# Performance work log

Hardware: AMD Instinct MI355X
Metric: run time of the kernel (lower is better)

The kernel has to match this reference:

```python
import jax, jax.numpy as jnp
import numpy as np

H = 256                      # latent_channels = LSTM hidden
OC = [32, 64, 64, 128]       # out_channels per mesh level
V = [5023, 1256, 314, 79, 20]  # vertex counts per level (fine -> coarse)
L = 9                        # spiral length
T = 64                       # audio frames (batch for decoder)


def setup_inputs() -> dict:
    key = jax.random.key(0)
    ks = iter(jax.random.split(key, 80))
    f32 = jnp.float32

    def nrm(shape, fan_in):
        return jax.random.normal(next(ks), shape, f32) * (1.0 / np.sqrt(fan_in))

    inp = {}
    inp['audio'] = jax.random.normal(next(ks), (T, 768), f32)
    inp['actor'] = jax.random.normal(next(ks), (V[0], 3), f32)

    # 5-layer bidirectional LSTM; layer 0 input 768, layers 1-4 input 2H
    inp['lstm_Wih0'] = nrm((2, 4 * H, 768), 768)
    inp['lstm_Whh0'] = nrm((2, 4 * H, H), H)
    inp['lstm_b0'] = jnp.zeros((2, 4 * H), f32)
    inp['lstm_Wih'] = nrm((4, 2, 4 * H, 2 * H), 2 * H)
    inp['lstm_Whh'] = nrm((4, 2, 4 * H, H), H)
    inp['lstm_b'] = jnp.zeros((4, 2, 4 * H), f32)

    # decoder entry fc: 2*latent -> num_vert * oc[-1]
    inp['fc_W'] = nrm((V[4] * OC[3], 2 * H), 2 * H)
    inp['fc_b'] = jnp.zeros((V[4] * OC[3],), f32)

    # SpiralConv weights (torch Linear layout: [out, in*L])
    inp['conv3_W'] = nrm((128, 128 * L), 128 * L); inp['conv3_b'] = jnp.zeros((128,), f32)
    inp['conv2_W'] = nrm((64, 128 * L), 128 * L);  inp['conv2_b'] = jnp.zeros((64,), f32)
    inp['conv1_W'] = nrm((64, 64 * L), 64 * L);    inp['conv1_b'] = jnp.zeros((64,), f32)
    inp['conv0_W'] = nrm((32, 64 * L), 64 * L);    inp['conv0_b'] = jnp.zeros((32,), f32)
    inp['head_W'] = nrm((3, 32 * L), 32 * L);      inp['head_b'] = jnp.zeros((3,), f32)

    # spiral indices per level: [V_j, L] with values in [0, V_j)
    for j in range(4):
        inp[f'idx{j}'] = jax.random.randint(next(ks), (V[j], L), 0, V[j], jnp.int32)

    # up_transform[j] sparse [V_j, V_{j+1}], ~3 nnz per row (COO)
    for j in range(4):
        nnz = 3 * V[j]
        inp[f'rows{j}'] = jnp.repeat(jnp.arange(V[j], dtype=jnp.int32), 3)
        inp[f'cols{j}'] = jax.random.randint(next(ks), (nnz,), 0, V[j + 1], jnp.int32)
        inp[f'vals{j}'] = jax.random.uniform(next(ks), (nnz,), f32) / 3.0
    return inp


def _lstm_dir(x, Wih, Whh, b, reverse):
    # x: [T, Din]; torch gate order i, f, g, o
    def step(carry, xt):
        h, c = carry
        g = Wih @ xt + Whh @ h + b            # [4H]
        i, f, gg, o = jnp.split(g, 4)
        c = jax.nn.sigmoid(f) * c + jax.nn.sigmoid(i) * jnp.tanh(gg)
        h = jax.nn.sigmoid(o) * jnp.tanh(c)
        return (h, c), h
    init = (jnp.zeros((H,), x.dtype), jnp.zeros((H,), x.dtype))
    _, hs = jax.lax.scan(step, init, x, reverse=reverse)
    return hs  # [T, H], aligned with input order


def _bilstm(x, Wih, Whh, b):
    hf = _lstm_dir(x, Wih[0], Whh[0], b[0], False)
    hb = _lstm_dir(x, Wih[1], Whh[1], b[1], True)
    return jnp.concatenate([hf, hb], axis=-1)  # [T, 2H]


def _pool(x, rows, cols, vals, n_out):
    # sparse up-transform: out[t, r] = sum_nnz vals * x[t, cols]
    g = x[:, cols, :] * vals[None, :, None]                       # [T, nnz, C]
    return jax.ops.segment_sum(g.swapaxes(0, 1), rows, num_segments=n_out).swapaxes(0, 1)


def _spiral(x, idx, W, b):
    # gather fixed spiral neighborhoods then dense linear
    g = x[:, idx, :].reshape(x.shape[0], idx.shape[0], -1)        # [T, V, L*C]
    return g @ W.T + b


def reference(audio, actor, lstm_Wih0, lstm_Whh0, lstm_b0, lstm_Wih, lstm_Whh, lstm_b,
              fc_W, fc_b, conv3_W, conv3_b, conv2_W, conv2_b, conv1_W, conv1_b,
              conv0_W, conv0_b, head_W, head_b,
              vals3, vals2, vals1, vals0,
              idx0, idx1, idx2, idx3,
              rows3, cols3, rows2, cols2, rows1, cols1, rows0, cols0):
    # audio embedding: 5-layer bidirectional LSTM (batch = 1)
    z = _bilstm(audio, lstm_Wih0, lstm_Whh0, lstm_b0)
    for l in range(4):
        z = _bilstm(z, lstm_Wih[l], lstm_Whh[l], lstm_b[l])       # [T, 2H]

    # decode
    x = (z @ fc_W.T + fc_b).reshape(z.shape[0], V[4], OC[3])      # [T, 20, 128]
    x = jax.nn.elu(_spiral(_pool(x, rows3, cols3, vals3, V[3]), idx3, conv3_W, conv3_b))
    x = jax.nn.elu(_spiral(_pool(x, rows2, cols2, vals2, V[2]), idx2, conv2_W, conv2_b))
    x = jax.nn.elu(_spiral(_pool(x, rows1, cols1, vals1, V[1]), idx1, conv1_W, conv1_b))
    x = jax.nn.elu(_spiral(_pool(x, rows0, cols0, vals0, V[0]), idx0, conv0_W, conv0_b))
    x = _spiral(x, idx0, head_W, head_b)                          # [T, 5023, 3]
    return x + actor[None]
```

## Files before the change

kernel.cpp:

```cpp
#include <hip/hip_runtime.h>
#include <hip/hip_bf16.h>

typedef __attribute__((ext_vector_type(8))) __bf16 bf16x8;
typedef __attribute__((ext_vector_type(4))) float  f32x4;
typedef __attribute__((ext_vector_type(4))) int    i32x4;

#define SCOPE_AGENT __HIP_MEMORY_SCOPE_AGENT

static __device__ __forceinline__ f32x4 mfma16(bf16x8 a, bf16x8 b, f32x4 c) {
    return __builtin_amdgcn_mfma_f32_16x16x32_bf16(a, b, c, 0, 0, 0);
}
static __device__ __forceinline__ i32x4 mfma_i8(i32x4 a, i32x4 b, i32x4 c) {
    return __builtin_amdgcn_mfma_i32_16x16x64_i8(a, b, c, 0, 0, 0);
}
static __device__ __forceinline__ float sigm(float x)  { return 1.0f / (1.0f + __expf(-x)); }
static __device__ __forceinline__ float tanh_(float x) { return 1.0f - 2.0f / (__expf(2.0f * x) + 1.0f); }

static __device__ __forceinline__ bf16x8 cvt8(const float* __restrict__ p) {
    const float4* q = (const float4*)p;
    float4 a = q[0], b = q[1];
    bf16x8 r;
    r[0] = (__bf16)a.x; r[1] = (__bf16)a.y; r[2] = (__bf16)a.z; r[3] = (__bf16)a.w;
    r[4] = (__bf16)b.x; r[5] = (__bf16)b.y; r[6] = (__bf16)b.z; r[7] = (__bf16)b.w;
    return r;
}
static __device__ __forceinline__ void signal_add(unsigned int* p) {
    __hip_atomic_fetch_add(p, 1u, __ATOMIC_RELEASE, SCOPE_AGENT);
}
template <int SLP>
static __device__ __forceinline__ void wait_eq(unsigned int* p, unsigned int v) {
    while (__hip_atomic_load(p, __ATOMIC_RELAXED, SCOPE_AGENT) != v)
        __builtin_amdgcn_s_sleep(SLP);
    (void)__hip_atomic_load(p, __ATOMIC_ACQUIRE, SCOPE_AGENT);
}
union g4u { unsigned long long q; __bf16 h[4]; };

#define ZBUF_OFF   1024
#define GX_OFF     132096
#define CONVW_OFF  66560
#define ARENA_A    621248
#define ARENA_B    21195456
#define WHHQ_BOFF  11534336
#define SWP_BOFF   14155776

__global__ __launch_bounds__(256) void precvt_whh(
    const float* __restrict__ Whh0, const float* __restrict__ WhhL,
    signed char* __restrict__ WhhQ, float* __restrict__ swp)
{
    const int g  = blockIdx.x * 4 + (threadIdx.x >> 6);
    const int dl = g >> 10;
    const int r  = g & 1023;
    const int lane = threadIdx.x & 63;
    const float* src = (dl < 2 ? Whh0 + (size_t)dl * 262144
                               : WhhL + (size_t)(dl - 2) * 262144) + (size_t)r * 256;
    float4 v = *(const float4*)(src + lane * 4);
    float am = fmaxf(fmaxf(fabsf(v.x), fabsf(v.y)), fmaxf(fabsf(v.z), fabsf(v.w)));
    #pragma unroll
    for (int m = 1; m < 64; m <<= 1) am = fmaxf(am, __shfl_xor(am, m));
    const float inv = am > 0.f ? 127.f / am : 0.f;
    int q0 = __float2int_rn(v.x * inv), q1 = __float2int_rn(v.y * inv);
    int q2 = __float2int_rn(v.z * inv), q3 = __float2int_rn(v.w * inv);
    unsigned pk = (q0 & 255) | ((q1 & 255) << 8) | ((q2 & 255) << 16) | ((q3 & 255) << 24);
    const int gate = r >> 8, cell = r & 255;
    const int m  = cell * 4 + gate;
    const int ln = m & 15, mt = m >> 4;
    const int k  = lane * 4;
    const int kc = k >> 6, quad = (k >> 4) & 3, j = k & 15;
    size_t addr = ((((size_t)dl * 64 + mt) * 4 + kc) * 64 + (quad * 16 + ln)) * 16 + j;
    *(unsigned*)(WhhQ + addr) = pk;
    if (lane == 0) swp[(size_t)dl * 1024 + cell * 4 + gate] = am / 127.f;
}

__global__ __launch_bounds__(256) void precvt_dec(
    const float* __restrict__ fcW, const float* __restrict__ c3W,
    const float* __restrict__ c2W, const float* __restrict__ c1W,
    const float* __restrict__ c0W, const float* __restrict__ hW,
    __bf16* __restrict__ fcWb, __bf16* __restrict__ convWb)
{
    int f = (blockIdx.x * 256 + threadIdx.x) * 4;
    if (f >= 1588064) return;
    const float* src; int off; __bf16* dst; int doff;
    if (f < 1310720) { src = fcW; off = f; dst = fcWb; doff = f; }
    else {
        int g = f - 1310720; dst = convWb; doff = g;
        if (g < 147456)      { src = c3W; off = g; }
        else if (g < 221184) { src = c2W; off = g - 147456; }
        else if (g < 258048) { src = c1W; off = g - 221184; }
        else if (g < 276480) { src = c0W; off = g - 258048; }
        else                 { src = hW;  off = g - 276480; }
    }
    float4 v = *(const float4*)(src + off);
    g4u u;
    u.h[0] = (__bf16)v.x; u.h[1] = (__bf16)v.y; u.h[2] = (__bf16)v.z; u.h[3] = (__bf16)v.w;
    *(unsigned long long*)(dst + doff) = u.q;
}

__global__ __launch_bounds__(512) __attribute__((amdgpu_waves_per_eu(2, 2)))
void lstm_fused(
    const float* __restrict__ audio,
    const float* __restrict__ Wih0,
    const float* __restrict__ WihL,
    const signed char* __restrict__ WhhQ,
    const float* __restrict__ swp,
    const float* __restrict__ b0, const float* __restrict__ bL,
    unsigned short* __restrict__ Gx_g,
    unsigned int* __restrict__ flags,
    unsigned short* __restrict__ zbuf)
{
    const int bid = blockIdx.x;
    const int tid = threadIdx.x;
    const int wave = tid >> 6, lane = tid & 63, ln = lane & 15, quad = lane >> 4;

    __shared__ __align__(16) signed char    hq[2][256];
    __shared__ __align__(16) unsigned short gx_l[16384];

    if (bid < 16) {
        const int dir = bid >> 3, sub = bid & 7;
        const int gmt = sub * 8 + wave;
        const int m_a = gmt * 16 + ln;
        const int r_a = (m_a & 3) * 256 + (m_a >> 2);
        unsigned short* GxO = Gx_g + (size_t)dir * 65536;

        {
            const float* Wih_l = Wih0 + (size_t)dir * 786432;
            const float* b_l   = b0 + (size_t)dir * 1024;
            bf16x8 afr[24];
            #pragma unroll
            for (int kc = 0; kc < 24; ++kc)
                afr[kc] = cvt8(Wih_l + (size_t)r_a * 768 + kc * 32 + quad * 8);
            float bv[4];
            #pragma unroll
            for (int reg = 0; reg < 4; ++reg) {
                const int m_row = gmt * 16 + quad * 4 + reg;
                bv[reg] = b_l[(m_row & 3) * 256 + (m_row >> 2)];
            }
            for (int ii = 0; ii < 4; ++ii) {
                const int nt = dir ? 3 - ii : ii;
                const int t  = nt * 16 + ln;
                f32x4 acA = (f32x4){0.f, 0.f, 0.f, 0.f};
                f32x4 acB = (f32x4){0.f, 0.f, 0.f, 0.f};
                #pragma unroll
                for (int kc = 0; kc < 24; kc += 2) {
                    acA = mfma16(afr[kc],
                                 cvt8(audio + (size_t)t * 768 + kc * 32 + quad * 8), acA);
                    acB = mfma16(afr[kc + 1],
                                 cvt8(audio + (size_t)t * 768 + (kc + 1) * 32 + quad * 8), acB);
                }
                f32x4 acc = acA + acB;
                #pragma unroll
                for (int reg = 0; reg < 4; ++reg) {
                    const int m_row = gmt * 16 + quad * 4 + reg;
                    __bf16 v = (__bf16)(acc[reg] + bv[reg]);
                    GxO[(size_t)t * 1024 + m_row] = __builtin_bit_cast(unsigned short, v);
                }
                __syncthreads();
                if (tid == 0) { __threadfence(); signal_add(&flags[(0 * 2 + dir) * 4 + nt]); }
            }
        }

        for (int l = 1; l < 5; ++l) {
            const float* Wih_l = WihL + (size_t)((l - 1) * 2 + dir) * 524288;
            const float* b_l   = bL + (size_t)((l - 1) * 2 + dir) * 1024;
            bf16x8 afr[16];
            #pragma unroll
            for (int kc = 0; kc < 16; ++kc)
                afr[kc] = cvt8(Wih_l + (size_t)r_a * 512 + kc * 32 + quad * 8);
            float bv[4];
            #pragma unroll
            for (int reg = 0; reg < 4; ++reg) {
                const int m_row = gmt * 16 + quad * 4 + reg;
                bv[reg] = b_l[(m_row & 3) * 256 + (m_row >> 2)];
            }
            if (tid == 0) wait_eq<4>(&flags[48 + (l - 1)], 2u);
            __syncthreads();
            const __bf16* zp = (const __bf16*)(zbuf + (size_t)((l - 1) & 1) * 32768);

            for (int ii = 0; ii < 4; ++ii) {
                const int nt = dir ? 3 - ii : ii;
                const int t  = nt * 16 + ln;
                f32x4 acA = (f32x4){0.f, 0.f, 0.f, 0.f};
                f32x4 acB = (f32x4){0.f, 0.f, 0.f, 0.f};
                #pragma unroll
                for (int kc = 0; kc < 16; kc += 2) {
                    acA = mfma16(afr[kc],
                                 *(const bf16x8*)(zp + (size_t)t * 512 + kc * 32 + quad * 8), acA);
                    acB = mfma16(afr[kc + 1],
                                 *(const bf16x8*)(zp + (size_t)t * 512 + (kc + 1) * 32 + quad * 8), acB);
                }
                f32x4 acc = acA + acB;
                #pragma unroll
                for (int reg = 0; reg < 4; ++reg) {
                    const int m_row = gmt * 16 + quad * 4 + reg;
                    __bf16 v = (__bf16)(acc[reg] + bv[reg]);
                    GxO[(size_t)t * 1024 + m_row] = __builtin_bit_cast(unsigned short, v);
                }
                __syncthreads();
                if (tid == 0) { __threadfence(); signal_add(&flags[(l * 2 + dir) * 4 + nt]); }
            }
        }
    } else {
        const int dir = bid - 16;
        const unsigned short* Gx_d = Gx_g + (size_t)dir * 65536;
        const bool owner = (ln < 8);
        const int cell = wave * 32 + ln * 4 + quad;
        const int gcell = owner ? cell : 0;
        const i32x4 czero = (i32x4){0, 0, 0, 0};

        for (int l = 0; l < 5; ++l) {
            const int dl = l * 2 + dir;
            i32x4 wf[8][4];
            const i32x4* wb = (const i32x4*)(WhhQ + (size_t)dl * 262144);
            #pragma unroll
            for (int i = 0; i < 8; ++i)
                #pragma unroll
                for (int kc = 0; kc < 4; ++kc)
                    wf[i][kc] = wb[(size_t)(((wave * 8 + i) * 4 + kc)) * 64 + lane];
            float sc0 = 0.f, sc1 = 0.f, sc2 = 0.f, sc3 = 0.f;
            if (owner) {
                float4 s4 = *(const float4*)(swp + (size_t)dl * 1024 + cell * 4);
                const float f = 1.f / 127.f;
                sc0 = s4.x * f; sc1 = s4.y * f; sc2 = s4.z * f; sc3 = s4.w * f;
            }
            if (tid < 64) ((unsigned int*)hq[0])[tid] = 0;
            float cst = 0.f;
            unsigned short* zl = zbuf + (size_t)(l & 1) * 32768;
            const int gxbase = (l * 2 + dir) * 4;

            for (int s = 0; s < 64; ++s) {
                if ((s & 15) == 0) {
                    const int nt = dir ? 3 - (s >> 4) : (s >> 4);
                    if (tid == 0) wait_eq<1>(&flags[gxbase + nt], 8u);
                    __syncthreads();
                    const float4* src = (const float4*)(Gx_d + (size_t)nt * 16384);
                    float4* dst = (float4*)gx_l;
                    #pragma unroll
                    for (int i = 0; i < 4; ++i) dst[i * 512 + tid] = src[i * 512 + tid];
                    __syncthreads();
                }
                const int t = dir ? (63 - s) : s;
                const int tl = t & 15;
                const int cur = s & 1, nxt = cur ^ 1;
                g4u gx;
                gx.q = *(const unsigned long long*)&gx_l[tl * 1024 + gcell * 4];
                i32x4 acc[8];
                {
                    i32x4 b0v = *(const i32x4*)&hq[cur][quad * 16];
                    #pragma unroll
                    for (int i = 0; i < 8; ++i) acc[i] = mfma_i8(wf[i][0], b0v, czero);
                }
                #pragma unroll
                for (int kc = 1; kc < 4; ++kc) {
                    i32x4 b = *(const i32x4*)&hq[cur][kc * 64 + quad * 16];
                    #pragma unroll
                    for (int i = 0; i < 8; ++i) acc[i] = mfma_i8(wf[i][kc], b, acc[i]);
                }
                i32x4 a = acc[0];
                #pragma unroll
                for (int j = 1; j < 8; ++j) if (ln == j) a = acc[j];
                if (owner) {
                    float gi = (float)a[0] * sc0 + (float)gx.h[0];
                    float gf = (float)a[1] * sc1 + (float)gx.h[1];
                    float gg = (float)a[2] * sc2 + (float)gx.h[2];
                    float go = (float)a[3] * sc3 + (float)gx.h[3];
                    cst = sigm(gf) * cst + sigm(gi) * tanh_(gg);
                    float h = sigm(go) * tanh_(cst);
                    int q = __float2int_rn(h * 127.f);
                    hq[nxt][cell] = (signed char)q;
                    __bf16 zv = (__bf16)((float)q * (1.f / 127.f));
                    zl[(size_t)t * 512 + dir * 256 + cell] =
                        __builtin_bit_cast(unsigned short, zv);
                }
                __syncthreads();
            }
            if (tid == 0) { __threadfence(); signal_add(&flags[48 + l]); }
        }
    }
}

__global__ __launch_bounds__(256) void fc_kernel(
    const __bf16* __restrict__ zb, const __bf16* __restrict__ W,
    const float* __restrict__ bb, __bf16* __restrict__ out)
{
    const int tid = threadIdx.x;
    const int wave = tid >> 6, lane = tid & 63, ln = lane & 15, quad = lane >> 4;
    const int nbase = blockIdx.x * 64;
    f32x4 acc[4];
    #pragma unroll
    for (int nt = 0; nt < 4; nt++) acc[nt] = (f32x4){0.f, 0.f, 0.f, 0.f};
    #pragma unroll 2
    for (int kc = 0; kc < 16; kc++) {
        const int k0 = kc * 32 + quad * 8;
        bf16x8 a = *(const bf16x8*)(zb + (size_t)(wave * 16 + ln) * 512 + k0);
        #pragma unroll
        for (int nt = 0; nt < 4; nt++) {
            bf16x8 b = *(const bf16x8*)(W + (size_t)(nbase + nt * 16 + ln) * 512 + k0);
            acc[nt] = mfma16(a, b, acc[nt]);
        }
    }
    #pragma unroll
    for (int nt = 0; nt < 4; nt++) {
        const int n = nbase + nt * 16 + ln;
        const float bv = bb[n];
        #pragma unroll
        for (int reg = 0; reg < 4; reg++) {
            const int t = wave * 16 + quad * 4 + reg;
            out[(size_t)((n >> 7) * 64 + t) * 128 + (n & 127)] = (__bf16)(acc[nt][reg] + bv);
        }
    }
}

template <int C>
__global__ __launch_bounds__(256) void pool_kernel(
    const __bf16* __restrict__ in, __bf16* __restrict__ out,
    const int* __restrict__ cols, const float* __restrict__ vals, int V)
{
    const int P = 64 * C / 8;
    const int gid = blockIdx.x * 256 + threadIdx.x;
    if (gid >= V * P) return;
    const int r = gid / P;
    const int rem = gid - r * P;
    float acc[8] = {0.f, 0.f, 0.f, 0.f, 0.f, 0.f, 0.f, 0.f};
    #pragma unroll
    for (int s = 0; s < 3; s++) {
        const int col = cols[3 * r + s];
        const float vv = vals[3 * r + s];
        bf16x8 x = *(const bf16x8*)(in + (size_t)col * 64 * C + rem * 8);
        #pragma unroll
        for (int e = 0; e < 8; e++) acc[e] += vv * (float)x[e];
    }
    bf16x8 ov;
    #pragma unroll
    for (int e = 0; e < 8; e++) ov[e] = (__bf16)acc[e];
    *(bf16x8*)(out + (size_t)r * 64 * C + rem * 8) = ov;
}

template <int CIN, int COUT>
__global__ __launch_bounds__(256) void conv_kernel(
    const __bf16* __restrict__ in, __bf16* __restrict__ out,
    const int* __restrict__ idx, const __bf16* __restrict__ W,
    const float* __restrict__ bias)
{
    constexpr int K = 9 * CIN;
    constexpr int NT = COUT / 16;
    constexpr int NKC = K / 32;
    const int v = blockIdx.x;
    const int tid = threadIdx.x;
    const int wave = tid >> 6, lane = tid & 63, ln = lane & 15, quad = lane >> 4;
    __shared__ int sIdx[9];
    if (tid < 9) sIdx[tid] = idx[v * 9 + tid];
    __syncthreads();
    f32x4 acc[NT];
    #pragma unroll
    for (int nt = 0; nt < NT; nt++) acc[nt] = (f32x4){0.f, 0.f, 0.f, 0.f};
    const int tt = wave * 16 + ln;
    for (int kc = 0; kc < NKC; kc++) {
        const int k0 = kc * 32;
        const int l = k0 / CIN;
        const int c = (k0 & (CIN - 1)) + quad * 8;
        const int row = sIdx[l];
        bf16x8 a = *(const bf16x8*)(in + ((size_t)row * 64 + tt) * CIN + c);
        #pragma unroll
        for (int nt = 0; nt < NT; nt++) {
            bf16x8 b = *(const bf16x8*)(W + (size_t)(nt * 16 + ln) * K + k0 + quad * 8);
            acc[nt] = mfma16(a, b, acc[nt]);
        }
    }
    #pragma unroll
    for (int nt = 0; nt < NT; nt++) {
        const int n = nt * 16 + ln;
        const float bv = bias[n];
        #pragma unroll
        for (int reg = 0; reg < 4; reg++) {
            const int t = wave * 16 + quad * 4 + reg;
            float val = acc[nt][reg] + bv;
            val = val > 0.f ? val : (__expf(val) - 1.f);
            out[((size_t)v * 64 + t) * COUT + n] = (__bf16)val;
        }
    }
}

__global__ __launch_bounds__(256) void head_kernel(
    const __bf16* __restrict__ in, float* __restrict__ out,
    const int* __restrict__ idx, const __bf16* __restrict__ W,
    const float* __restrict__ bias, const float* __restrict__ actor)
{
    const int v = blockIdx.x;
    const int tid = threadIdx.x;
    const int wave = tid >> 6, lane = tid & 63, ln = lane & 15, quad = lane >> 4;
    __shared__ int sIdx[9];
    if (tid < 9) sIdx[tid] = idx[v * 9 + tid];
    __syncthreads();
    f32x4 acc = (f32x4){0.f, 0.f, 0.f, 0.f};
    const int tt = wave * 16 + ln;
    const int rown = ln < 3 ? ln : 0;
    #pragma unroll
    for (int kc = 0; kc < 9; kc++) {
        const int row = sIdx[kc];
        bf16x8 a = *(const bf16x8*)(in + ((size_t)row * 64 + tt) * 32 + quad * 8);
        bf16x8 b = *(const bf16x8*)(W + (size_t)rown * 288 + kc * 32 + quad * 8);
        acc = mfma16(a, b, acc);
    }
    if (ln < 3) {
        const float bv = bias[ln];
        const float av = actor[v * 3 + ln];
        #pragma unroll
        for (int reg = 0; reg < 4; reg++) {
            const int t = wave * 16 + quad * 4 + reg;
            out[((size_t)t * 5023 + v) * 3 + ln] = acc[reg] + bv + av;
        }
    }
}

extern "C" void kernel_launch(void* const* d_in, const int* in_sizes, int n_in,
                              void* d_out, int out_size, void* d_ws, size_t ws_size,
                              hipStream_t stream) {
    const float* audio = (const float*)d_in[0];
    const float* actor = (const float*)d_in[1];
    const float* Wih0  = (const float*)d_in[2];
    const float* Whh0  = (const float*)d_in[3];
    const float* b0    = (const float*)d_in[4];
    const float* WihL  = (const float*)d_in[5];
    const float* WhhL  = (const float*)d_in[6];
    const float* bLs   = (const float*)d_in[7];
    const float* fcW   = (const float*)d_in[8];
    const float* fcb   = (const float*)d_in[9];
    const float* c3W = (const float*)d_in[10]; const float* c3b = (const float*)d_in[11];
    const float* c2W = (const float*)d_in[12]; const float* c2b = (const float*)d_in[13];
    const float* c1W = (const float*)d_in[14]; const float* c1b = (const float*)d_in[15];
    const float* c0W = (const float*)d_in[16]; const float* c0b = (const float*)d_in[17];
    const float* hW  = (const float*)d_in[18]; const float* hb  = (const float*)d_in[19];
    const int* idx0 = (const int*)d_in[20];
    const int* idx1 = (const int*)d_in[21];
    const int* idx2 = (const int*)d_in[22];
    const int* idx3 = (const int*)d_in[23];
    const int* cols0 = (const int*)d_in[25]; const float* vals0 = (const float*)d_in[26];
    const int* cols1 = (const int*)d_in[28]; const float* vals1 = (const float*)d_in[29];
    const int* cols2 = (const int*)d_in[31]; const float* vals2 = (const float*)d_in[32];
    const int* cols3 = (const int*)d_in[34]; const float* vals3 = (const float*)d_in[35];

    char* ws = (char*)d_ws;
    unsigned int*   flags = (unsigned int*)ws;
    unsigned short* zbuf  = (unsigned short*)(ws + ZBUF_OFF);
    unsigned short* GxG   = (unsigned short*)(ws + GX_OFF);
    __bf16*         convWb = (__bf16*)(ws + CONVW_OFF);
    char* arenaA = ws + ARENA_A;
    char* arenaB = ws + ARENA_B;

    signed char* whhq = (signed char*)(arenaB + WHHQ_BOFF);
    float*       swp  = (float*)(arenaB + SWP_BOFF);
    __bf16*      fcWb = (__bf16*)(arenaB + 2097152);

    __bf16* x4b = (__bf16*)arenaA;
    __bf16* p3  = (__bf16*)arenaB;
    __bf16* c3o = (__bf16*)arenaA;
    __bf16* p2  = (__bf16*)arenaB;
    __bf16* c2o = (__bf16*)arenaA;
    __bf16* p1  = (__bf16*)arenaB;
    __bf16* c1o = (__bf16*)arenaA;
    __bf16* p0  = (__bf16*)arenaB;
    __bf16* c0o = (__bf16*)arenaA;

    (void)hipMemsetAsync(ws, 0, 1024, stream);

    precvt_whh<<<2560, 256, 0, stream>>>(Whh0, WhhL, whhq, swp);
    lstm_fused<<<18, 512, 0, stream>>>(audio, Wih0, WihL, whhq, swp, b0, bLs,
                                       GxG, flags, zbuf);
    precvt_dec<<<1552, 256, 0, stream>>>(fcW, c3W, c2W, c1W, c0W, hW, fcWb, convWb);

    fc_kernel<<<40, 256, 0, stream>>>((const __bf16*)zbuf, fcWb, fcb, x4b);

    { int n = 79 * 64 * 128 / 8;
      pool_kernel<128><<<(n + 255) / 256, 256, 0, stream>>>(x4b, p3, cols3, vals3, 79);
      conv_kernel<128, 128><<<79, 256, 0, stream>>>(p3, c3o, idx3, convWb + 0, c3b); }
    { int n = 314 * 64 * 128 / 8;
      pool_kernel<128><<<(n + 255) / 256, 256, 0, stream>>>(c3o, p2, cols2, vals2, 314);
      conv_kernel<128, 64><<<314, 256, 0, stream>>>(p2, c2o, idx2, convWb + 147456, c2b); }
    { int n = 1256 * 64 * 64 / 8;
      pool_kernel<64><<<(n + 255) / 256, 256, 0, stream>>>(c2o, p1, cols1, vals1, 1256);
      conv_kernel<64, 64><<<1256, 256, 0, stream>>>(p1, c1o, idx1, convWb + 221184, c1b); }
    { int n = 5023 * 64 * 64 / 8;
      pool_kernel<64><<<(n + 255) / 256, 256, 0, stream>>>(c1o, p0, cols0, vals0, 5023);
      conv_kernel<64, 32><<<5023, 256, 0, stream>>>(p0, c0o, idx0, convWb + 258048, c0b); }

    head_kernel<<<5023, 256, 0, stream>>>(c0o, (float*)d_out, idx0, convWb + 276480, hb, actor);
}
```

Before: 851.9 us.

## Fuse weight precast into LSTM launch and pool into spiral conv

Folds the Whh int8 quantisation and the decoder bf16 conversion into extra blocks of the LSTM launch. The recurrent blocks wait on a flag for the quantised weights, and the decoder conversion runs alongside the serial recurrence. The four pool kernels are fused into the spiral conv kernels, which gather the 3 sparse up-sample contributions per spiral neighbour directly, removing the pooled intermediate buffers. It also drops the LDS staging of Gx in the recurrent loop and reads it from global memory instead. The trade-offs are 3x redundant gather loads in the conv and possibly extra latency on the recurrent path.

```diff
diff --git a/kernel.cpp b/kernel.cpp
--- a/kernel.cpp
+++ b/kernel.cpp
@@ -37,72 +37,28 @@
 
 #define ZBUF_OFF   1024
 #define GX_OFF     132096
-#define CONVW_OFF  66560
 #define ARENA_A    621248
 #define ARENA_B    21195456
 #define WHHQ_BOFF  11534336
 #define SWP_BOFF   14155776
-
-__global__ __launch_bounds__(256) void precvt_whh(
-    const float* __restrict__ Whh0, const float* __restrict__ WhhL,
-    signed char* __restrict__ WhhQ, float* __restrict__ swp)
-{
-    const int g  = blockIdx.x * 4 + (threadIdx.x >> 6);
-    const int dl = g >> 10;
-    const int r  = g & 1023;
-    const int lane = threadIdx.x & 63;
-    const float* src = (dl < 2 ? Whh0 + (size_t)dl * 262144
-                               : WhhL + (size_t)(dl - 2) * 262144) + (size_t)r * 256;
-    float4 v = *(const float4*)(src + lane * 4);
-    float am = fmaxf(fmaxf(fabsf(v.x), fabsf(v.y)), fmaxf(fabsf(v.z), fabsf(v.w)));
-    #pragma unroll
-    for (int m = 1; m < 64; m <<= 1) am = fmaxf(am, __shfl_xor(am, m));
-    const float inv = am > 0.f ? 127.f / am : 0.f;
-    int q0 = __float2int_rn(v.x * inv), q1 = __float2int_rn(v.y * inv);
-    int q2 = __float2int_rn(v.z * inv), q3 = __float2int_rn(v.w * inv);
-    unsigned pk = (q0 & 255) | ((q1 & 255) << 8) | ((q2 & 255) << 16) | ((q3 & 255) << 24);
-    const int gate = r >> 8, cell = r & 255;
-    const int m  = cell * 4 + gate;
-    const int ln = m & 15, mt = m >> 4;
-    const int k  = lane * 4;
-    const int kc = k >> 6, quad = (k >> 4) & 3, j = k & 15;
-    size_t addr = ((((size_t)dl * 64 + mt) * 4 + kc) * 64 + (quad * 16 + ln)) * 16 + j;
-    *(unsigned*)(WhhQ + addr) = pk;
-    if (lane == 0) swp[(size_t)dl * 1024 + cell * 4 + gate] = am / 127.f;
-}
-
-__global__ __launch_bounds__(256) void precvt_dec(
-    const float* __restrict__ fcW, const float* __restrict__ c3W,
-    const float* __restrict__ c2W, const float* __restrict__ c1W,
-    const float* __restrict__ c0W, const float* __restrict__ hW,
-    __bf16* __restrict__ fcWb, __bf16* __restrict__ convWb)
-{
-    int f = (blockIdx.x * 256 + threadIdx.x) * 4;
-    if (f >= 1588064) return;
-    const float* src; int off; __bf16* dst; int doff;
-    if (f < 1310720) { src = fcW; off = f; dst = fcWb; doff = f; }
-    else {
-        int g = f - 1310720; dst = convWb; doff = g;
-        if (g < 147456)      { src = c3W; off = g; }
-        else if (g < 221184) { src = c2W; off = g - 147456; }
-        else if (g < 258048) { src = c1W; off = g - 221184; }
-        else if (g < 276480) { src = c0W; off = g - 258048; }
-        else                 { src = hW;  off = g - 276480; }
-    }
-    float4 v = *(const float4*)(src + off);
-    g4u u;
-    u.h[0] = (__bf16)v.x; u.h[1] = (__bf16)v.y; u.h[2] = (__bf16)v.z; u.h[3] = (__bf16)v.w;
-    *(unsigned long long*)(dst + doff) = u.q;
-}
+#define CONVW_BOFF 16777216
+
+#define NB_LSTM 18
+#define NB_WHH  1280
+#define NB_DEC  776
 
 __global__ __launch_bounds__(512) __attribute__((amdgpu_waves_per_eu(2, 2)))
 void lstm_fused(
     const float* __restrict__ audio,
     const float* __restrict__ Wih0,
     const float* __restrict__ WihL,
-    const signed char* __restrict__ WhhQ,
-    const float* __restrict__ swp,
+    const float* __restrict__ Whh0, const float* __restrict__ WhhL,
+    signed char* __restrict__ WhhQ, float* __restrict__ swp,
     const float* __restrict__ b0, const float* __restrict__ bL,
+    const float* __restrict__ fcW, const float* __restrict__ c3W,
+    const float* __restrict__ c2W, const float* __restrict__ c1W,
+    const float* __restrict__ c0W, const float* __restrict__ hW,
+    __bf16* __restrict__ fcWb, __bf16* __restrict__ convWb,
     unsigned short* __restrict__ Gx_g,
     unsigned int* __restrict__ flags,
     unsigned short* __restrict__ zbuf)
@@ -111,8 +67,55 @@
     const int tid = threadIdx.x;
     const int wave = tid >> 6, lane = tid & 63, ln = lane & 15, quad = lane >> 4;
 
-    __shared__ __align__(16) signed char    hq[2][256];
-    __shared__ __align__(16) unsigned short gx_l[16384];
+    __shared__ __align__(16) signed char hq[2][256];
+
+    if (bid >= NB_LSTM) {
+        if (bid < NB_LSTM + NB_WHH) {
+            const int g  = (bid - NB_LSTM) * 8 + wave;
+            const int dl = g >> 10;
+            const int r  = g & 1023;
+            const float* src = (dl < 2 ? Whh0 + (size_t)dl * 262144
+                                       : WhhL + (size_t)(dl - 2) * 262144) + (size_t)r * 256;
+            float4 v = *(const float4*)(src + lane * 4);
+            float am = fmaxf(fmaxf(fabsf(v.x), fabsf(v.y)), fmaxf(fabsf(v.z), fabsf(v.w)));
+            #pragma unroll
+            for (int m = 1; m < 64; m <<= 1) am = fmaxf(am, __shfl_xor(am, m));
+            const float inv = am > 0.f ? 127.f / am : 0.f;
+            int q0 = __float2int_rn(v.x * inv), q1 = __float2int_rn(v.y * inv);
+            int q2 = __float2int_rn(v.z * inv), q3 = __float2int_rn(v.w * inv);
+            unsigned pk = (q0 & 255) | ((q1 & 255) << 8) | ((q2 & 255) << 16) | ((q3 & 255) << 24);
+            const int gate = r >> 8, cell = r & 255;
+            const int m  = cell * 4 + gate;
+            const int lm = m & 15, mt = m >> 4;
+            const int k  = lane * 4;
+            const int kc = k >> 6, qd = (k >> 4) & 3, j = k & 15;
+            size_t addr = ((((size_t)dl * 64 + mt) * 4 + kc) * 64 + (qd * 16 + lm)) * 16 + j;
+            *(unsigned*)(WhhQ + addr) = pk;
+            if (lane == 0) swp[(size_t)dl * 1024 + cell * 4 + gate] = am / 127.f;
+            __syncthreads();
+            if (tid == 0) { __threadfence(); signal_add(&flags[60]); }
+        } else {
+            int f = ((bid - NB_LSTM - NB_WHH) * 512 + tid) * 4;
+            if (f < 1588064) {
+                const float* src; int off; __bf16* dst; int doff;
+                if (f < 1310720) { src = fcW; off = f; dst = fcWb; doff = f; }
+                else {
+                    int g = f - 1310720; dst = convWb; doff = g;
+                    if (g < 147456)      { src = c3W; off = g; }
+                    else if (g < 221184) { src = c2W; off = g - 147456; }
+                    else if (g < 258048) { src = c1W; off = g - 221184; }
+                    else if (g < 276480) { src = c0W; off = g - 258048; }
+                    else                 { src = hW;  off = g - 276480; }
+                }
+                float4 v = *(const float4*)(src + off);
+                g4u u;
+                u.h[0] = (__bf16)v.x; u.h[1] = (__bf16)v.y;
+                u.h[2] = (__bf16)v.z; u.h[3] = (__bf16)v.w;
+                *(unsigned long long*)(dst + doff) = u.q;
+            }
+        }
+        return;
+    }
 
     if (bid < 16) {
         const int dir = bid >> 3, sub = bid & 7;
@@ -206,6 +209,9 @@
         const int gcell = owner ? cell : 0;
         const i32x4 czero = (i32x4){0, 0, 0, 0};
 
+        if (tid == 0) wait_eq<4>(&flags[60], (unsigned)NB_WHH);
+        __syncthreads();
+
         for (int l = 0; l < 5; ++l) {
             const int dl = l * 2 + dir;
             i32x4 wf[8][4];
@@ -231,17 +237,11 @@
                     const int nt = dir ? 3 - (s >> 4) : (s >> 4);
                     if (tid == 0) wait_eq<1>(&flags[gxbase + nt], 8u);
                     __syncthreads();
-                    const float4* src = (const float4*)(Gx_d + (size_t)nt * 16384);
-                    float4* dst = (float4*)gx_l;
-                    #pragma unroll
-                    for (int i = 0; i < 4; ++i) dst[i * 512 + tid] = src[i * 512 + tid];
-                    __syncthreads();
                 }
                 const int t = dir ? (63 - s) : s;
-                const int tl = t & 15;
                 const int cur = s & 1, nxt = cur ^ 1;
                 g4u gx;
-                gx.q = *(const unsigned long long*)&gx_l[tl * 1024 + gcell * 4];
+                gx.q = *(const unsigned long long*)(Gx_d + (size_t)t * 1024 + gcell * 4);
                 i32x4 acc[8];
                 {
                     i32x4 b0v = *(const i32x4*)&hq[cur][quad * 16];
@@ -309,36 +309,12 @@
     }
 }
 
-template <int C>
-__global__ __launch_bounds__(256) void pool_kernel(
+template <int CIN, int COUT>
+__global__ __launch_bounds__(256) void convpool_kernel(
     const __bf16* __restrict__ in, __bf16* __restrict__ out,
-    const int* __restrict__ cols, const float* __restrict__ vals, int V)
-{
-    const int P = 64 * C / 8;
-    const int gid = blockIdx.x * 256 + threadIdx.x;
-    if (gid >= V * P) return;
-    const int r = gid / P;
-    const int rem = gid - r * P;
-    float acc[8] = {0.f, 0.f, 0.f, 0.f, 0.f, 0.f, 0.f, 0.f};
-    #pragma unroll
-    for (int s = 0; s < 3; s++) {
-        const int col = cols[3 * r + s];
-        const float vv = vals[3 * r + s];
-        bf16x8 x = *(const bf16x8*)(in + (size_t)col * 64 * C + rem * 8);
-        #pragma unroll
-        for (int e = 0; e < 8; e++) acc[e] += vv * (float)x[e];
-    }
-    bf16x8 ov;
-    #pragma unroll
-    for (int e = 0; e < 8; e++) ov[e] = (__bf16)acc[e];
-    *(bf16x8*)(out + (size_t)r * 64 * C + rem * 8) = ov;
-}
-
-template <int CIN, int COUT>
-__global__ __launch_bounds__(256) void conv_kernel(
-    const __bf16* __restrict__ in, __bf16* __restrict__ out,
-    const int* __restrict__ idx, const __bf16* __restrict__ W,
-    const float* __restrict__ bias)
+    const int* __restrict__ idx,
+    const int* __restrict__ cols, const float* __restrict__ vals,
+    const __bf16* __restrict__ W, const float* __restrict__ bias)
 {
     constexpr int K = 9 * CIN;
     constexpr int NT = COUT / 16;
@@ -346,8 +322,14 @@
     const int v = blockIdx.x;
     const int tid = threadIdx.x;
     const int wave = tid >> 6, lane = tid & 63, ln = lane & 15, quad = lane >> 4;
-    __shared__ int sIdx[9];
-    if (tid < 9) sIdx[tid] = idx[v * 9 + tid];
+    __shared__ int   sCol[27];
+    __shared__ float sVal[27];
+    if (tid < 27) {
+        const int l = tid / 3, s = tid - l * 3;
+        const int r = idx[v * 9 + l];
+        sCol[tid] = cols[3 * r + s];
+        sVal[tid] = vals[3 * r + s];
+    }
     __syncthreads();
     f32x4 acc[NT];
     #pragma unroll
@@ -357,8 +339,18 @@
         const int k0 = kc * 32;
         const int l = k0 / CIN;
         const int c = (k0 & (CIN - 1)) + quad * 8;
-        const int row = sIdx[l];
-        bf16x8 a = *(const bf16x8*)(in + ((size_t)row * 64 + tt) * CIN + c);
+        float af[8] = {0.f, 0.f, 0.f, 0.f, 0.f, 0.f, 0.f, 0.f};
+        #pragma unroll
+        for (int s = 0; s < 3; s++) {
+            const int col = sCol[l * 3 + s];
+            const float vv = sVal[l * 3 + s];
+            bf16x8 x = *(const bf16x8*)(in + ((size_t)col * 64 + tt) * CIN + c);
+            #pragma unroll
+            for (int e = 0; e < 8; e++) af[e] += vv * (float)x[e];
+        }
+        bf16x8 a;
+        #pragma unroll
+        for (int e = 0; e < 8; e++) a[e] = (__bf16)af[e];
         #pragma unroll
         for (int nt = 0; nt < NT; nt++) {
             bf16x8 b = *(const bf16x8*)(W + (size_t)(nt * 16 + ln) * K + k0 + quad * 8);
@@ -442,45 +434,37 @@
     unsigned int*   flags = (unsigned int*)ws;
     unsigned short* zbuf  = (unsigned short*)(ws + ZBUF_OFF);
     unsigned short* GxG   = (unsigned short*)(ws + GX_OFF);
-    __bf16*         convWb = (__bf16*)(ws + CONVW_OFF);
     char* arenaA = ws + ARENA_A;
     char* arenaB = ws + ARENA_B;
 
     signed char* whhq = (signed char*)(arenaB + WHHQ_BOFF);
     float*       swp  = (float*)(arenaB + SWP_BOFF);
     __bf16*      fcWb = (__bf16*)(arenaB + 2097152);
+    __bf16*     convWb = (__bf16*)(arenaB + CONVW_BOFF);
 
     __bf16* x4b = (__bf16*)arenaA;
-    __bf16* p3  = (__bf16*)arenaB;
-    __bf16* c3o = (__bf16*)arenaA;
-    __bf16* p2  = (__bf16*)arenaB;
+    __bf16* c3o = (__bf16*)arenaB;
     __bf16* c2o = (__bf16*)arenaA;
-    __bf16* p1  = (__bf16*)arenaB;
-    __bf16* c1o = (__bf16*)arenaA;
-    __bf16* p0  = (__bf16*)arenaB;
+    __bf16* c1o = (__bf16*)arenaB;
     __bf16* c0o = (__bf16*)arenaA;
 
     (void)hipMemsetAsync(ws, 0, 1024, stream);
 
-    precvt_whh<<<2560, 256, 0, stream>>>(Whh0, WhhL, whhq, swp);
-    lstm_fused<<<18, 512, 0, stream>>>(audio, Wih0, WihL, whhq, swp, b0, bLs,
-                                       GxG, flags, zbuf);
-    precvt_dec<<<1552, 256, 0, stream>>>(fcW, c3W, c2W, c1W, c0W, hW, fcWb, convWb);
+    lstm_fused<<<NB_LSTM + NB_WHH + NB_DEC, 512, 0, stream>>>(
+        audio, Wih0, WihL, Whh0, WhhL, whhq, swp, b0, bLs,
+        fcW, c3W, c2W, c1W, c0W, hW, fcWb, convWb,
+        GxG, flags, zbuf);
 
     fc_kernel<<<40, 256, 0, stream>>>((const __bf16*)zbuf, fcWb, fcb, x4b);
 
-    { int n = 79 * 64 * 128 / 8;
-      pool_kernel<128><<<(n + 255) / 256, 256, 0, stream>>>(x4b, p3, cols3, vals3, 79);
-      conv_kernel<128, 128><<<79, 256, 0, stream>>>(p3, c3o, idx3, convWb + 0, c3b); }
-    { int n = 314 * 64 * 128 / 8;
-      pool_kernel<128><<<(n + 255) / 256, 256, 0, stream>>>(c3o, p2, cols2, vals2, 314);
-      conv_kernel<128, 64><<<314, 256, 0, stream>>>(p2, c2o, idx2, convWb + 147456, c2b); }
-    { int n = 1256 * 64 * 64 / 8;
-      pool_kernel<64><<<(n + 255) / 256, 256, 0, stream>>>(c2o, p1, cols1, vals1, 1256);
-      conv_kernel<64, 64><<<1256, 256, 0, stream>>>(p1, c1o, idx1, convWb + 221184, c1b); }
-    { int n = 5023 * 64 * 64 / 8;
-      pool_kernel<64><<<(n + 255) / 256, 256, 0, stream>>>(c1o, p0, cols0, vals0, 5023);
-      conv_kernel<64, 32><<<5023, 256, 0, stream>>>(p0, c0o, idx0, convWb + 258048, c0b); }
+    convpool_kernel<128, 128><<<79, 256, 0, stream>>>(x4b, c3o, idx3, cols3, vals3,
+                                                      convWb + 0, c3b);
+    convpool_kernel<128, 64><<<314, 256, 0, stream>>>(c3o, c2o, idx2, cols2, vals2,
+                                                      convWb + 147456, c2b);
+    convpool_kernel<64, 64><<<1256, 256, 0, stream>>>(c2o, c1o, idx1, cols1, vals1,
+                                                      convWb + 221184, c1b);
+    convpool_kernel<64, 32><<<5023, 256, 0, stream>>>(c1o, c0o, idx0, cols0, vals0,
+                                                      convWb + 258048, c0b);
 
     head_kernel<<<5023, 256, 0, stream>>>(c0o, (float*)d_out, idx0, convWb + 276480, hb, actor);
 }
```

Result: slower. 1.034 ms (+21.4%).

## Fold weight pre-conversion into LSTM and fc launches; split conv blocks per wave

Applied to the files above, without the earlier changes.

Removes the separate Whh quantisation and decoder weight conversion kernels. Their work moves into extra blocks of the fused LSTM kernel and the fc kernel. The recurrent LSTM blocks spin on a new flag counter until all Whh quantisation blocks finish, and the fc weight conversion now overlaps the LSTM recurrence. Conv and head kernels switch from 256-thread blocks to 64-thread blocks over a 2D grid, one wave per 16-frame slice. This cuts launch count and overlaps conversion with the serial LSTM, but relies on co-residency of the spinning and converting blocks, and the spiral index loads are now repeated per wave.

```diff
diff --git a/kernel.cpp b/kernel.cpp
--- a/kernel.cpp
+++ b/kernel.cpp
@@ -43,66 +43,19 @@
 #define WHHQ_BOFF  11534336
 #define SWP_BOFF   14155776
 
-__global__ __launch_bounds__(256) void precvt_whh(
-    const float* __restrict__ Whh0, const float* __restrict__ WhhL,
-    signed char* __restrict__ WhhQ, float* __restrict__ swp)
-{
-    const int g  = blockIdx.x * 4 + (threadIdx.x >> 6);
-    const int dl = g >> 10;
-    const int r  = g & 1023;
-    const int lane = threadIdx.x & 63;
-    const float* src = (dl < 2 ? Whh0 + (size_t)dl * 262144
-                               : WhhL + (size_t)(dl - 2) * 262144) + (size_t)r * 256;
-    float4 v = *(const float4*)(src + lane * 4);
-    float am = fmaxf(fmaxf(fabsf(v.x), fabsf(v.y)), fmaxf(fabsf(v.z), fabsf(v.w)));
-    #pragma unroll
-    for (int m = 1; m < 64; m <<= 1) am = fmaxf(am, __shfl_xor(am, m));
-    const float inv = am > 0.f ? 127.f / am : 0.f;
-    int q0 = __float2int_rn(v.x * inv), q1 = __float2int_rn(v.y * inv);
-    int q2 = __float2int_rn(v.z * inv), q3 = __float2int_rn(v.w * inv);
-    unsigned pk = (q0 & 255) | ((q1 & 255) << 8) | ((q2 & 255) << 16) | ((q3 & 255) << 24);
-    const int gate = r >> 8, cell = r & 255;
-    const int m  = cell * 4 + gate;
-    const int ln = m & 15, mt = m >> 4;
-    const int k  = lane * 4;
-    const int kc = k >> 6, quad = (k >> 4) & 3, j = k & 15;
-    size_t addr = ((((size_t)dl * 64 + mt) * 4 + kc) * 64 + (quad * 16 + ln)) * 16 + j;
-    *(unsigned*)(WhhQ + addr) = pk;
-    if (lane == 0) swp[(size_t)dl * 1024 + cell * 4 + gate] = am / 127.f;
-}
-
-__global__ __launch_bounds__(256) void precvt_dec(
-    const float* __restrict__ fcW, const float* __restrict__ c3W,
-    const float* __restrict__ c2W, const float* __restrict__ c1W,
-    const float* __restrict__ c0W, const float* __restrict__ hW,
-    __bf16* __restrict__ fcWb, __bf16* __restrict__ convWb)
-{
-    int f = (blockIdx.x * 256 + threadIdx.x) * 4;
-    if (f >= 1588064) return;
-    const float* src; int off; __bf16* dst; int doff;
-    if (f < 1310720) { src = fcW; off = f; dst = fcWb; doff = f; }
-    else {
-        int g = f - 1310720; dst = convWb; doff = g;
-        if (g < 147456)      { src = c3W; off = g; }
-        else if (g < 221184) { src = c2W; off = g - 147456; }
-        else if (g < 258048) { src = c1W; off = g - 221184; }
-        else if (g < 276480) { src = c0W; off = g - 258048; }
-        else                 { src = hW;  off = g - 276480; }
-    }
-    float4 v = *(const float4*)(src + off);
-    g4u u;
-    u.h[0] = (__bf16)v.x; u.h[1] = (__bf16)v.y; u.h[2] = (__bf16)v.z; u.h[3] = (__bf16)v.w;
-    *(unsigned long long*)(dst + doff) = u.q;
-}
+#define NB_LSTM 18
+#define NB_WHH  1280
+#define NB_FCW  640
 
 __global__ __launch_bounds__(512) __attribute__((amdgpu_waves_per_eu(2, 2)))
 void lstm_fused(
     const float* __restrict__ audio,
     const float* __restrict__ Wih0,
     const float* __restrict__ WihL,
-    const signed char* __restrict__ WhhQ,
-    const float* __restrict__ swp,
+    const float* __restrict__ Whh0, const float* __restrict__ WhhL,
+    signed char* __restrict__ WhhQ, float* __restrict__ swp,
     const float* __restrict__ b0, const float* __restrict__ bL,
+    const float* __restrict__ fcW, __bf16* __restrict__ fcWb,
     unsigned short* __restrict__ Gx_g,
     unsigned int* __restrict__ flags,
     unsigned short* __restrict__ zbuf)
@@ -113,6 +66,44 @@
 
     __shared__ __align__(16) signed char    hq[2][256];
     __shared__ __align__(16) unsigned short gx_l[16384];
+
+    if (bid >= NB_LSTM) {
+        if (bid < NB_LSTM + NB_WHH) {
+            const int g  = (bid - NB_LSTM) * 8 + wave;
+            const int dl = g >> 10;
+            const int r  = g & 1023;
+            const float* src = (dl < 2 ? Whh0 + (size_t)dl * 262144
+                                       : WhhL + (size_t)(dl - 2) * 262144) + (size_t)r * 256;
+            float4 v = *(const float4*)(src + lane * 4);
+            float am = fmaxf(fmaxf(fabsf(v.x), fabsf(v.y)), fmaxf(fabsf(v.z), fabsf(v.w)));
+            #pragma unroll
+            for (int m = 1; m < 64; m <<= 1) am = fmaxf(am, __shfl_xor(am, m));
+            const float inv = am > 0.f ? 127.f / am : 0.f;
+            int q0 = __float2int_rn(v.x * inv), q1 = __float2int_rn(v.y * inv);
+            int q2 = __float2int_rn(v.z * inv), q3 = __float2int_rn(v.w * inv);
+            unsigned pk = (q0 & 255) | ((q1 & 255) << 8) | ((q2 & 255) << 16) | ((q3 & 255) << 24);
+            const int gate = r >> 8, cell = r & 255;
+            const int m  = cell * 4 + gate;
+            const int lm = m & 15, mt = m >> 4;
+            const int k  = lane * 4;
+            const int kc = k >> 6, qd = (k >> 4) & 3, j = k & 15;
+            size_t addr = ((((size_t)dl * 64 + mt) * 4 + kc) * 64 + (qd * 16 + lm)) * 16 + j;
+            *(unsigned*)(WhhQ + addr) = pk;
+            if (lane == 0) swp[(size_t)dl * 1024 + cell * 4 + gate] = am / 127.f;
+            __syncthreads();
+            if (tid == 0) { __threadfence(); signal_add(&flags[60]); }
+        } else {
+            int f = ((bid - NB_LSTM - NB_WHH) * 512 + tid) * 4;
+            if (f < 1310720) {
+                float4 v = *(const float4*)(fcW + f);
+                g4u u;
+                u.h[0] = (__bf16)v.x; u.h[1] = (__bf16)v.y;
+                u.h[2] = (__bf16)v.z; u.h[3] = (__bf16)v.w;
+                *(unsigned long long*)(fcWb + f) = u.q;
+            }
+        }
+        return;
+    }
 
     if (bid < 16) {
         const int dir = bid >> 3, sub = bid & 7;
@@ -205,6 +196,9 @@
         const int cell = wave * 32 + ln * 4 + quad;
         const int gcell = owner ? cell : 0;
         const i32x4 czero = (i32x4){0, 0, 0, 0};
+
+        if (tid == 0) wait_eq<4>(&flags[60], (unsigned)NB_WHH);
+        __syncthreads();
 
         for (int l = 0; l < 5; ++l) {
             const int dl = l * 2 + dir;
@@ -279,9 +273,29 @@
 
 __global__ __launch_bounds__(256) void fc_kernel(
     const __bf16* __restrict__ zb, const __bf16* __restrict__ W,
-    const float* __restrict__ bb, __bf16* __restrict__ out)
+    const float* __restrict__ bb, __bf16* __restrict__ out,
+    const float* __restrict__ c3W, const float* __restrict__ c2W,
+    const float* __restrict__ c1W, const float* __restrict__ c0W,
+    const float* __restrict__ hW, __bf16* __restrict__ convWb)
 {
     const int tid = threadIdx.x;
+    if (blockIdx.x >= 40) {
+        int f = ((blockIdx.x - 40) * 256 + tid) * 4;
+        if (f < 277344) {
+            const float* src; int off;
+            if (f < 147456)      { src = c3W; off = f; }
+            else if (f < 221184) { src = c2W; off = f - 147456; }
+            else if (f < 258048) { src = c1W; off = f - 221184; }
+            else if (f < 276480) { src = c0W; off = f - 258048; }
+            else                 { src = hW;  off = f - 276480; }
+            float4 v = *(const float4*)(src + off);
+            g4u u;
+            u.h[0] = (__bf16)v.x; u.h[1] = (__bf16)v.y;
+            u.h[2] = (__bf16)v.z; u.h[3] = (__bf16)v.w;
+            *(unsigned long long*)(convWb + f) = u.q;
+        }
+        return;
+    }
     const int wave = tid >> 6, lane = tid & 63, ln = lane & 15, quad = lane >> 4;
     const int nbase = blockIdx.x * 64;
     f32x4 acc[4];
@@ -335,7 +349,7 @@
 }
 
 template <int CIN, int COUT>
-__global__ __launch_bounds__(256) void conv_kernel(
+__global__ __launch_bounds__(64) void conv_kernel(
     const __bf16* __restrict__ in, __bf16* __restrict__ out,
     const int* __restrict__ idx, const __bf16* __restrict__ W,
     const float* __restrict__ bias)
@@ -344,15 +358,15 @@
     constexpr int NT = COUT / 16;
     constexpr int NKC = K / 32;
     const int v = blockIdx.x;
-    const int tid = threadIdx.x;
-    const int wave = tid >> 6, lane = tid & 63, ln = lane & 15, quad = lane >> 4;
+    const int lane = threadIdx.x, ln = lane & 15, quad = lane >> 4;
+    const int t0 = blockIdx.y * 16;
     __shared__ int sIdx[9];
-    if (tid < 9) sIdx[tid] = idx[v * 9 + tid];
+    if (lane < 9) sIdx[lane] = idx[v * 9 + lane];
     __syncthreads();
     f32x4 acc[NT];
     #pragma unroll
     for (int nt = 0; nt < NT; nt++) acc[nt] = (f32x4){0.f, 0.f, 0.f, 0.f};
-    const int tt = wave * 16 + ln;
+    const int tt = t0 + ln;
     for (int kc = 0; kc < NKC; kc++) {
         const int k0 = kc * 32;
         const int l = k0 / CIN;
@@ -371,7 +385,7 @@
         const float bv = bias[n];
         #pragma unroll
         for (int reg = 0; reg < 4; reg++) {
-            const int t = wave * 16 + quad * 4 + reg;
+            const int t = t0 + quad * 4 + reg;
             float val = acc[nt][reg] + bv;
             val = val > 0.f ? val : (__expf(val) - 1.f);
             out[((size_t)v * 64 + t) * COUT + n] = (__bf16)val;
@@ -379,19 +393,19 @@
     }
 }
 
-__global__ __launch_bounds__(256) void head_kernel(
+__global__ __launch_bounds__(64) void head_kernel(
     const __bf16* __restrict__ in, float* __restrict__ out,
     const int* __restrict__ idx, const __bf16* __restrict__ W,
     const float* __restrict__ bias, const float* __restrict__ actor)
 {
     const int v = blockIdx.x;
-    const int tid = threadIdx.x;
-    const int wave = tid >> 6, lane = tid & 63, ln = lane & 15, quad = lane >> 4;
+    const int lane = threadIdx.x, ln = lane & 15, quad = lane >> 4;
+    const int t0 = blockIdx.y * 16;
     __shared__ int sIdx[9];
-    if (tid < 9) sIdx[tid] = idx[v * 9 + tid];
+    if (lane < 9) sIdx[lane] = idx[v * 9 + lane];
     __syncthreads();
     f32x4 acc = (f32x4){0.f, 0.f, 0.f, 0.f};
-    const int tt = wave * 16 + ln;
+    const int tt = t0 + ln;
     const int rown = ln < 3 ? ln : 0;
     #pragma unroll
     for (int kc = 0; kc < 9; kc++) {
@@ -405,7 +419,7 @@
         const float av = actor[v * 3 + ln];
         #pragma unroll
         for (int reg = 0; reg < 4; reg++) {
-            const int t = wave * 16 + quad * 4 + reg;
+            const int t = t0 + quad * 4 + reg;
             out[((size_t)t * 5023 + v) * 3 + ln] = acc[reg] + bv + av;
         }
     }
@@ -462,25 +476,26 @@
 
     (void)hipMemsetAsync(ws, 0, 1024, stream);
 
-    precvt_whh<<<2560, 256, 0, stream>>>(Whh0, WhhL, whhq, swp);
-    lstm_fused<<<18, 512, 0, stream>>>(audio, Wih0, WihL, whhq, swp, b0, bLs,
-                                       GxG, flags, zbuf);
-    precvt_dec<<<1552, 256, 0, stream>>>(fcW, c3W, c2W, c1W, c0W, hW, fcWb, convWb);
-
-    fc_kernel<<<40, 256, 0, stream>>>((const __bf16*)zbuf, fcWb, fcb, x4b);
+    lstm_fused<<<NB_LSTM + NB_WHH + NB_FCW, 512, 0, stream>>>(
+        audio, Wih0, WihL, Whh0, WhhL, whhq, swp, b0, bLs,
+        fcW, fcWb, GxG, flags, zbuf);
+
+    fc_kernel<<<40 + 271, 256, 0, stream>>>((const __bf16*)zbuf, fcWb, fcb, x4b,
+                                            c3W, c2W, c1W, c0W, hW, convWb);
 
     { int n = 79 * 64 * 128 / 8;
       pool_kernel<128><<<(n + 255) / 256, 256, 0, stream>>>(x4b, p3, cols3, vals3, 79);
-      conv_kernel<128, 128><<<79, 256, 0, stream>>>(p3, c3o, idx3, convWb + 0, c3b); }
+      conv_kernel<128, 128><<<dim3(79, 4), 64, 0, stream>>>(p3, c3o, idx3, convWb + 0, c3b); }
     { int n = 314 * 64 * 128 / 8;
       pool_kernel<128><<<(n + 255) / 256, 256, 0, stream>>>(c3o, p2, cols2, vals2, 314);
-      conv_kernel<128, 64><<<314, 256, 0, stream>>>(p2, c2o, idx2, convWb + 147456, c2b); }
+      conv_kernel<128, 64><<<dim3(314, 4), 64, 0, stream>>>(p2, c2o, idx2, convWb + 147456, c2b); }
     { int n = 1256 * 64 * 64 / 8;
       pool_kernel<64><<<(n + 255) / 256, 256, 0, stream>>>(c2o, p1, cols1, vals1, 1256);
-      conv_kernel<64, 64><<<1256, 256, 0, stream>>>(p1, c1o, idx1, convWb + 221184, c1b); }
+      conv_kernel<64, 64><<<dim3(1256, 4), 64, 0, stream>>>(p1, c1o, idx1, convWb + 221184, c1b); }
     { int n = 5023 * 64 * 64 / 8;
       pool_kernel<64><<<(n + 255) / 256, 256, 0, stream>>>(c1o, p0, cols0, vals0, 5023);
-      conv_kernel<64, 32><<<5023, 256, 0, stream>>>(p0, c0o, idx0, convWb + 258048, c0b); }
-
-    head_kernel<<<5023, 256, 0, stream>>>(c0o, (float*)d_out, idx0, convWb + 276480, hb, actor);
-}
+      conv_kernel<64, 32><<<dim3(5023, 4), 64, 0, stream>>>(p0, c0o, idx0, convWb + 258048, c0b); }
+
+    head_kernel<<<dim3(5023, 4), 64, 0, stream>>>(c0o, (float*)d_out, idx0,
+                                                  convWb + 276480, hb, actor);
+}
```

After: 866.7 us. Within noise of the previous version (+1.7%).
